# Performance work log

Measured on AMD Instinct MI355X. Metric: run time of the kernel, lower is better.

Reference implementation:

```python
import jax, jax.numpy as jnp
import numpy as np


def setup_inputs() -> dict:
    key = jax.random.key(0)
    kx, ky = jax.random.split(key)
    x = jax.random.normal(kx, (8, 4096, 3), dtype=jnp.float32)
    y = jax.random.normal(ky, (8, 4096, 3), dtype=jnp.float32)
    return {"x": x, "y": y}


def reference(x, y):
    # Mathematically identical to sum((x[:, :, None] - y[:, None, :])**2, -1)
    # but avoids materializing the [B, n, m, 3] diff tensor.
    x2 = jnp.sum(x * x, axis=-1)              # [B, n]
    y2 = jnp.sum(y * y, axis=-1)              # [B, m]
    xy = jnp.einsum('bnd,bmd->bnm', x, y)     # [B, n, m]
    dist = x2[:, :, None] + y2[:, None, :] - 2.0 * xy  # [B, n, m]
    min_dist_xy = jnp.min(dist, axis=2)       # [B, n] nearest y for each x
    min_dist_yx = jnp.min(dist, axis=1)       # [B, m] nearest x for each y
    return jnp.mean(min_dist_xy, axis=1) + jnp.mean(min_dist_yx, axis=1)  # [B]
```

## Files before the change

kernel.cpp:

```cpp
#include <hip/hip_runtime.h>
#include <math.h>

#define BLK 256
#define NX 16
#define NPTS 4096
#define YLEN 128
#define CCH (NPTS / YLEN)
#define UNITS 65536

__global__ __launch_bounds__(BLK, 2) void chamfer_partial_kernel(
    const float* __restrict__ X, const float* __restrict__ Y,
    float* __restrict__ partial, float* __restrict__ out)
{
  __shared__ float4 sh[YLEN];

  int lin = blockIdx.x;
  int c   = lin % CCH; lin /= CCH;
  int b   = lin & 7;
  int dir = lin >> 3;

  const float* xs = (dir ? Y : X) + b * (NPTS * 3);
  const float* ys = (dir ? X : Y) + b * (NPTS * 3);

  if (blockIdx.x == 0 && threadIdx.x < 8) out[threadIdx.x] = 0.0f;

  int ybase = c * YLEN;
  if (threadIdx.x < YLEN) {
    int j = threadIdx.x;
    float y0 = ys[(ybase + j) * 3 + 0];
    float y1 = ys[(ybase + j) * 3 + 1];
    float y2 = ys[(ybase + j) * 3 + 2];
    sh[j] = make_float4(y0, y1, y2, 0.5f * (y0 * y0 + y1 * y1 + y2 * y2));
  }
  __syncthreads();

  int x0i = threadIdx.x * NX;
  float xf[NX * 3];
  {
    const float4* xp = reinterpret_cast<const float4*>(xs + x0i * 3);
    #pragma unroll
    for (int i = 0; i < 12; ++i) {
      float4 p = xp[i];
      xf[i * 4 + 0] = p.x; xf[i * 4 + 1] = p.y;
      xf[i * 4 + 2] = p.z; xf[i * 4 + 3] = p.w;
    }
  }
  float n0[NX], n1[NX], n2[NX], x2h[NX], gm[NX];
  #pragma unroll
  for (int k = 0; k < NX; ++k) {
    float a = xf[k * 3 + 0], bb = xf[k * 3 + 1], cc = xf[k * 3 + 2];
    n0[k] = -a; n1[k] = -bb; n2[k] = -cc;
    x2h[k] = 0.5f * (a * a + bb * bb + cc * cc);
    gm[k] = __builtin_inff();
  }

  auto proc = [&](const float4& p0, const float4& p1,
                  const float4& p2, const float4& p3) {
    #pragma unroll
    for (int k = 0; k < NX; ++k) {
      float ga = fmaf(n0[k], p0.x, fmaf(n1[k], p0.y, fmaf(n2[k], p0.z, p0.w)));
      float gb = fmaf(n0[k], p1.x, fmaf(n1[k], p1.y, fmaf(n2[k], p1.z, p1.w)));
      float gc = fmaf(n0[k], p2.x, fmaf(n1[k], p2.y, fmaf(n2[k], p2.z, p2.w)));
      float gd = fmaf(n0[k], p3.x, fmaf(n1[k], p3.y, fmaf(n2[k], p3.z, p3.w)));
      float m  = fminf(fminf(ga, gb), gc);
      gm[k] = fminf(fminf(m, gd), gm[k]);
    }
  };

  float4 c0 = sh[0], c1 = sh[1], c2 = sh[2], c3 = sh[3];
  #pragma unroll 2
  for (int j = 4; j < YLEN; j += 4) {
    float4 t0 = sh[j], t1 = sh[j + 1], t2 = sh[j + 2], t3 = sh[j + 3];
    proc(c0, c1, c2, c3);
    c0 = t0; c1 = t1; c2 = t2; c3 = t3;
  }
  proc(c0, c1, c2, c3);

  float* dst = partial + (size_t)c * UNITS + dir * 32768 + b * 4096 + x0i;
  float4* d4 = reinterpret_cast<float4*>(dst);
  #pragma unroll
  for (int q = 0; q < 4; ++q)
    d4[q] = make_float4(2.0f * (x2h[q * 4 + 0] + gm[q * 4 + 0]),
                        2.0f * (x2h[q * 4 + 1] + gm[q * 4 + 1]),
                        2.0f * (x2h[q * 4 + 2] + gm[q * 4 + 2]),
                        2.0f * (x2h[q * 4 + 3] + gm[q * 4 + 3]));
}

__global__ __launch_bounds__(BLK, 4) void chamfer_reduce_kernel(
    const float* __restrict__ partial, float* __restrict__ out, int C)
{
  int b = blockIdx.x >> 5;
  int s = blockIdx.x & 31;
  int i = s * BLK + threadIdx.x;
  int dir = i >> 12;
  int xi  = i & 4095;
  int unit = dir * 32768 + b * 4096 + xi;
  float v0 = __builtin_inff(), v1 = v0, v2 = v0, v3 = v0;
  int c = 0;
  for (; c + 4 <= C; c += 4) {
    v0 = fminf(v0, partial[(size_t)(c + 0) * UNITS + unit]);
    v1 = fminf(v1, partial[(size_t)(c + 1) * UNITS + unit]);
    v2 = fminf(v2, partial[(size_t)(c + 2) * UNITS + unit]);
    v3 = fminf(v3, partial[(size_t)(c + 3) * UNITS + unit]);
  }
  for (; c < C; ++c) v0 = fminf(v0, partial[(size_t)c * UNITS + unit]);
  float v = fminf(fminf(v0, v1), fminf(v2, v3));
  #pragma unroll
  for (int off = 32; off > 0; off >>= 1) v += __shfl_down(v, off, 64);
  __shared__ float wsum[BLK / 64];
  if ((threadIdx.x & 63) == 0) wsum[threadIdx.x >> 6] = v;
  __syncthreads();
  if (threadIdx.x == 0) {
    float t = wsum[0] + wsum[1] + wsum[2] + wsum[3];
    atomicAdd(&out[b], t * (1.0f / 4096.0f));
  }
}

__global__ __launch_bounds__(BLK, 2) void chamfer_direct_kernel(
    const float* __restrict__ X, const float* __restrict__ Y,
    float* __restrict__ out)
{
  extern __shared__ float4 shd[];
  int lin = blockIdx.x;
  int xt  = lin & 1;  lin >>= 1;
  int b   = lin & 7;
  int dir = lin >> 3;
  const float* xs = (dir ? Y : X) + b * (NPTS * 3);
  const float* ys = (dir ? X : Y) + b * (NPTS * 3);

  for (int j = threadIdx.x; j < NPTS; j += BLK) {
    float y0 = ys[j * 3 + 0], y1 = ys[j * 3 + 1], y2 = ys[j * 3 + 2];
    shd[j] = make_float4(y0, y1, y2, 0.5f * (y0 * y0 + y1 * y1 + y2 * y2));
  }
  __syncthreads();

  int x0i = xt * (BLK * 8) + threadIdx.x * 8;
  float xf[24];
  const float4* xp = reinterpret_cast<const float4*>(xs + x0i * 3);
  #pragma unroll
  for (int i = 0; i < 6; ++i) {
    float4 p = xp[i];
    xf[i * 4 + 0] = p.x; xf[i * 4 + 1] = p.y;
    xf[i * 4 + 2] = p.z; xf[i * 4 + 3] = p.w;
  }
  float n0[8], n1[8], n2[8], x2h[8], gm[8];
  #pragma unroll
  for (int k = 0; k < 8; ++k) {
    float a = xf[k * 3 + 0], bb = xf[k * 3 + 1], cc = xf[k * 3 + 2];
    n0[k] = -a; n1[k] = -bb; n2[k] = -cc;
    x2h[k] = 0.5f * (a * a + bb * bb + cc * cc);
    gm[k] = __builtin_inff();
  }
  for (int j = 0; j < NPTS; j += 4) {
    float4 p0 = shd[j], p1 = shd[j + 1], p2 = shd[j + 2], p3 = shd[j + 3];
    #pragma unroll
    for (int k = 0; k < 8; ++k) {
      float ga = fmaf(n0[k], p0.x, fmaf(n1[k], p0.y, fmaf(n2[k], p0.z, p0.w)));
      float gb = fmaf(n0[k], p1.x, fmaf(n1[k], p1.y, fmaf(n2[k], p1.z, p1.w)));
      float gc = fmaf(n0[k], p2.x, fmaf(n1[k], p2.y, fmaf(n2[k], p2.z, p2.w)));
      float gd = fmaf(n0[k], p3.x, fmaf(n1[k], p3.y, fmaf(n2[k], p3.z, p3.w)));
      float m  = fminf(fminf(ga, gb), gc);
      gm[k] = fminf(fminf(m, gd), gm[k]);
    }
  }
  float v = 0.0f;
  #pragma unroll
  for (int k = 0; k < 8; ++k) v += 2.0f * (x2h[k] + gm[k]);
  #pragma unroll
  for (int off = 32; off > 0; off >>= 1) v += __shfl_down(v, off, 64);
  __syncthreads();
  float* red = reinterpret_cast<float*>(shd);
  if ((threadIdx.x & 63) == 0) red[threadIdx.x >> 6] = v;
  __syncthreads();
  if (threadIdx.x == 0) {
    float s = red[0] + red[1] + red[2] + red[3];
    atomicAdd(&out[b], s * (1.0f / 4096.0f));
  }
}

__global__ void zero_out_kernel(float* out)
{
  if (threadIdx.x < 8) out[threadIdx.x] = 0.0f;
}

extern "C" void kernel_launch(void* const* d_in, const int* in_sizes, int n_in,
                              void* d_out, int out_size, void* d_ws, size_t ws_size,
                              hipStream_t stream)
{
  const float* X = (const float*)d_in[0];
  const float* Y = (const float*)d_in[1];
  float* out = (float*)d_out;

  if (ws_size >= (size_t)CCH * UNITS * sizeof(float)) {
    chamfer_partial_kernel<<<2 * 8 * CCH, BLK, 0, stream>>>(
        X, Y, (float*)d_ws, out);
    chamfer_reduce_kernel<<<256, BLK, 0, stream>>>((const float*)d_ws, out, CCH);
  } else {
    zero_out_kernel<<<1, 64, 0, stream>>>(out);
    chamfer_direct_kernel<<<2 * 8 * 2, BLK, NPTS * sizeof(float4), stream>>>(
        X, Y, out);
  }
}
```

Baseline: 83.88 us.

## Retile partial kernel to 8 x-points per thread with 256-point y chunks

```diff
diff --git a/kernel.cpp b/kernel.cpp
--- a/kernel.cpp
+++ b/kernel.cpp
@@ -2,9 +2,10 @@
 #include <math.h>
 
 #define BLK 256
-#define NX 16
+#define NX 8
+#define XT 2
 #define NPTS 4096
-#define YLEN 128
+#define YLEN 256
 #define CCH (NPTS / YLEN)
 #define UNITS 65536
 
@@ -16,6 +17,7 @@
 
   int lin = blockIdx.x;
   int c   = lin % CCH; lin /= CCH;
+  int xt  = lin % XT;  lin /= XT;
   int b   = lin & 7;
   int dir = lin >> 3;
 
@@ -24,22 +26,21 @@
 
   if (blockIdx.x == 0 && threadIdx.x < 8) out[threadIdx.x] = 0.0f;
 
-  int ybase = c * YLEN;
-  if (threadIdx.x < YLEN) {
+  {
     int j = threadIdx.x;
-    float y0 = ys[(ybase + j) * 3 + 0];
-    float y1 = ys[(ybase + j) * 3 + 1];
-    float y2 = ys[(ybase + j) * 3 + 2];
+    float y0 = ys[(c * YLEN + j) * 3 + 0];
+    float y1 = ys[(c * YLEN + j) * 3 + 1];
+    float y2 = ys[(c * YLEN + j) * 3 + 2];
     sh[j] = make_float4(y0, y1, y2, 0.5f * (y0 * y0 + y1 * y1 + y2 * y2));
   }
   __syncthreads();
 
-  int x0i = threadIdx.x * NX;
+  int x0i = xt * (BLK * NX) + threadIdx.x * NX;
   float xf[NX * 3];
   {
     const float4* xp = reinterpret_cast<const float4*>(xs + x0i * 3);
     #pragma unroll
-    for (int i = 0; i < 12; ++i) {
+    for (int i = 0; i < 6; ++i) {
       float4 p = xp[i];
       xf[i * 4 + 0] = p.x; xf[i * 4 + 1] = p.y;
       xf[i * 4 + 2] = p.z; xf[i * 4 + 3] = p.w;
@@ -54,8 +55,9 @@
     gm[k] = __builtin_inff();
   }
 
-  auto proc = [&](const float4& p0, const float4& p1,
-                  const float4& p2, const float4& p3) {
+  #pragma unroll 4
+  for (int j = 0; j < YLEN; j += 4) {
+    float4 p0 = sh[j], p1 = sh[j + 1], p2 = sh[j + 2], p3 = sh[j + 3];
     #pragma unroll
     for (int k = 0; k < NX; ++k) {
       float ga = fmaf(n0[k], p0.x, fmaf(n1[k], p0.y, fmaf(n2[k], p0.z, p0.w)));
@@ -65,29 +67,18 @@
       float m  = fminf(fminf(ga, gb), gc);
       gm[k] = fminf(fminf(m, gd), gm[k]);
     }
-  };
-
-  float4 c0 = sh[0], c1 = sh[1], c2 = sh[2], c3 = sh[3];
-  #pragma unroll 2
-  for (int j = 4; j < YLEN; j += 4) {
-    float4 t0 = sh[j], t1 = sh[j + 1], t2 = sh[j + 2], t3 = sh[j + 3];
-    proc(c0, c1, c2, c3);
-    c0 = t0; c1 = t1; c2 = t2; c3 = t3;
   }
-  proc(c0, c1, c2, c3);
 
   float* dst = partial + (size_t)c * UNITS + dir * 32768 + b * 4096 + x0i;
   float4* d4 = reinterpret_cast<float4*>(dst);
-  #pragma unroll
-  for (int q = 0; q < 4; ++q)
-    d4[q] = make_float4(2.0f * (x2h[q * 4 + 0] + gm[q * 4 + 0]),
-                        2.0f * (x2h[q * 4 + 1] + gm[q * 4 + 1]),
-                        2.0f * (x2h[q * 4 + 2] + gm[q * 4 + 2]),
-                        2.0f * (x2h[q * 4 + 3] + gm[q * 4 + 3]));
+  d4[0] = make_float4(2.0f * (x2h[0] + gm[0]), 2.0f * (x2h[1] + gm[1]),
+                      2.0f * (x2h[2] + gm[2]), 2.0f * (x2h[3] + gm[3]));
+  d4[1] = make_float4(2.0f * (x2h[4] + gm[4]), 2.0f * (x2h[5] + gm[5]),
+                      2.0f * (x2h[6] + gm[6]), 2.0f * (x2h[7] + gm[7]));
 }
 
 __global__ __launch_bounds__(BLK, 4) void chamfer_reduce_kernel(
-    const float* __restrict__ partial, float* __restrict__ out, int C)
+    const float* __restrict__ partial, float* __restrict__ out)
 {
   int b = blockIdx.x >> 5;
   int s = blockIdx.x & 31;
@@ -96,15 +87,20 @@
   int xi  = i & 4095;
   int unit = dir * 32768 + b * 4096 + xi;
   float v0 = __builtin_inff(), v1 = v0, v2 = v0, v3 = v0;
-  int c = 0;
-  for (; c + 4 <= C; c += 4) {
+  float v4 = v0, v5 = v0, v6 = v0, v7 = v0;
+  #pragma unroll
+  for (int c = 0; c < CCH; c += 8) {
     v0 = fminf(v0, partial[(size_t)(c + 0) * UNITS + unit]);
     v1 = fminf(v1, partial[(size_t)(c + 1) * UNITS + unit]);
     v2 = fminf(v2, partial[(size_t)(c + 2) * UNITS + unit]);
     v3 = fminf(v3, partial[(size_t)(c + 3) * UNITS + unit]);
+    v4 = fminf(v4, partial[(size_t)(c + 4) * UNITS + unit]);
+    v5 = fminf(v5, partial[(size_t)(c + 5) * UNITS + unit]);
+    v6 = fminf(v6, partial[(size_t)(c + 6) * UNITS + unit]);
+    v7 = fminf(v7, partial[(size_t)(c + 7) * UNITS + unit]);
   }
-  for (; c < C; ++c) v0 = fminf(v0, partial[(size_t)c * UNITS + unit]);
-  float v = fminf(fminf(v0, v1), fminf(v2, v3));
+  float v = fminf(fminf(fminf(v0, v1), fminf(v2, v3)),
+                  fminf(fminf(v4, v5), fminf(v6, v7)));
   #pragma unroll
   for (int off = 32; off > 0; off >>= 1) v += __shfl_down(v, off, 64);
   __shared__ float wsum[BLK / 64];
@@ -192,9 +188,9 @@
   float* out = (float*)d_out;
 
   if (ws_size >= (size_t)CCH * UNITS * sizeof(float)) {
-    chamfer_partial_kernel<<<2 * 8 * CCH, BLK, 0, stream>>>(
+    chamfer_partial_kernel<<<2 * 8 * XT * CCH, BLK, 0, stream>>>(
         X, Y, (float*)d_ws, out);
-    chamfer_reduce_kernel<<<256, BLK, 0, stream>>>((const float*)d_ws, out, CCH);
+    chamfer_reduce_kernel<<<256, BLK, 0, stream>>>((const float*)d_ws, out);
   } else {
     zero_out_kernel<<<1, 64, 0, stream>>>(out);
     chamfer_direct_kernel<<<2 * 8 * 2, BLK, NPTS * sizeof(float4), stream>>>(
```

Result: faster. 80.71 us (median of 2 runs) (-3.8%).
